# Performance work log

Hardware: AMD Instinct MI355X
Metric: run time of the kernel (lower is better)

## Reference

```python
import jax, jax.numpy as jnp
import numpy as np

W_CUB = 0.1
W_CD = 1.0
W_EXT = 0.01
W_SPS = 0.01
THRED = 24.0
COS_EPS = 1e-4

# cube face buffers (6 faces x 3 coords)
MASK_PROJECT = jnp.array([[0,1,1],[0,1,1],[1,0,1],[1,0,1],[1,1,0],[1,1,0]], jnp.float32)
MASK_PLANE   = jnp.array([[1,0,0],[1,0,0],[0,1,0],[0,1,0],[0,0,1],[0,0,1]], jnp.float32)
CUBE_NORMAL  = jnp.array([[-1,0,0],[1,0,0],[0,-1,0],[0,1,0],[0,0,-1],[0,0,1]], jnp.float32)
# torch repeat(...,3,...) of [[-1,-1,-1],[1,1,1]] tiles it -> [c0,c1,c0,c1,c0,c1]
CUBE_PLANES6 = jnp.tile(jnp.array([[-1.,-1.,-1.],[1.,1.,1.]], jnp.float32), (3,1))


def setup_inputs():
    B, P, N, S = 4, 24, 3072, 128
    key = jax.random.key(0)
    ks = jax.random.split(key, 8)
    pc_inver = jax.random.normal(ks[0], (B, P, N, 3), jnp.float32)
    normals_inver = jax.random.normal(ks[1], (B, P, N, 3), jnp.float32)
    scale = jax.random.uniform(ks[2], (B, P, 3), jnp.float32) * 0.9 + 0.1
    shape = jax.random.uniform(ks[3], (B, P, 2), jnp.float32) * 1.3 + 0.2
    exist = jax.random.uniform(ks[4], (B, P, 1), jnp.float32) * 0.98 + 0.01
    assign_matrix = jax.nn.softmax(jax.random.normal(ks[5], (B, N, P), jnp.float32), axis=-1)
    etas = jax.random.uniform(ks[6], (B, P, S), jnp.float32, minval=-jnp.pi/2, maxval=jnp.pi/2)
    omegas = jax.random.uniform(ks[7], (B, P, S), jnp.float32, minval=-jnp.pi, maxval=jnp.pi)
    return dict(pc_inver=pc_inver, normals_inver=normals_inver, scale=scale,
                shape=shape, exist=exist, assign_matrix=assign_matrix,
                etas=etas, omegas=omegas)


def _fexp(x, p):
    return jnp.sign(x) * jnp.abs(x) ** p


def _sample_sq_points(scale, eps, etas, omegas):
    # scale (B,P,3), eps (B,P,2), etas/omegas (B,P,S) -> (B,P,S,3)
    etas = jnp.where(etas == 0, 1e-6, etas)
    omegas = jnp.where(omegas == 0, 1e-6, omegas)
    a1, a2, a3 = scale[..., 0:1], scale[..., 1:2], scale[..., 2:3]
    e1, e2 = eps[..., 0:1], eps[..., 1:2]
    ce, se = jnp.cos(etas), jnp.sin(etas)
    co, so = jnp.cos(omegas), jnp.sin(omegas)
    x = a1 * _fexp(ce, e1) * _fexp(co, e2)
    y = a2 * _fexp(ce, e1) * _fexp(so, e2)
    z = a3 * _fexp(se, e1)
    fix = lambda v: (jnp.where(v > 0, 1.0, -1.0)) * jnp.maximum(jnp.abs(v), 1e-6)
    return jnp.stack([fix(x), fix(y), fix(z)], -1)


def _cd_loss(pc_inver, scale, shape, exist, assign_matrix, etas, omegas):
    X = _sample_sq_points(scale, shape, etas, omegas)          # (B,P,S,3)
    diff = X[:, :, :, None, :] - pc_inver[:, :, None, :, :]    # (B,P,S,N,3)
    D = jnp.sum(diff * diff, -1)                               # (B,P,S,N)
    pcl2prim = jnp.min(D, axis=2)                              # (B,P,N)
    pcl_loss = jnp.mean(jnp.sum(jnp.swapaxes(pcl2prim, 1, 2) * assign_matrix, -1))
    prim2pcl = jnp.mean(jnp.min(D, axis=3), axis=-1)           # (B,P)
    e = exist[..., 0]
    prim_loss = jnp.mean(jnp.sum(prim2pcl * e, -1) / (jnp.sum(e, -1) + 1e-6))
    return pcl_loss, prim_loss


def _cuboid_loss(pc_inver, normals_inver, scale, assign_matrix):
    pc = jnp.swapaxes(pc_inver, 1, 2)        # (B,N,P,3)
    nrm = jnp.swapaxes(normals_inver, 1, 2)  # (B,N,P,3)
    n_norm = jnp.maximum(jnp.linalg.norm(nrm, axis=-1, keepdims=True), COS_EPS)
    cos = jnp.einsum('bnpc,fc->bnpf', nrm, CUBE_NORMAL) / n_norm  # ||cube_normal||=1
    idx = jnp.argmax(cos, axis=-1)           # (B,N,P)
    s = scale[:, None, :, None, :]           # (B,1,P,1,3)
    proj = pc[:, :, :, None, :] * MASK_PROJECT + (CUBE_PLANES6 * s) * MASK_PLANE  # (B,N,P,6,3)
    proj = jnp.clip(proj, -s, s)
    proj_sel = jnp.take_along_axis(proj, idx[..., None, None], axis=3)[..., 0, :]  # (B,N,P,3)
    d = jnp.sum((proj_sel - pc) ** 2, -1)    # (B,N,P)
    return jnp.mean(jnp.sum(d * assign_matrix, -1))


def _common_losses(assign_matrix, exist):
    gt = jax.lax.stop_gradient((jnp.sum(assign_matrix, 1) > THRED).astype(jnp.float32))  # (B,P)
    p = exist[..., 0]
    bce = -jnp.mean(gt * jnp.log(p) + (1.0 - gt) * jnp.log1p(-p))
    N = assign_matrix.shape[1]
    sps = jnp.mean(jnp.mean(jnp.sqrt(jnp.sum(assign_matrix, 1) / N + 0.01), -1) ** 2)
    return bce, sps


def reference(pc_inver, normals_inver, scale, shape, exist, assign_matrix, etas, omegas):
    cub = _cuboid_loss(pc_inver, normals_inver, scale, assign_matrix)
    pcl_loss, prim_loss = _cd_loss(pc_inver, scale, shape, exist, assign_matrix, etas, omegas)
    bce, sps = _common_losses(assign_matrix, exist)
    return W_CUB * cub + W_CD * (pcl_loss + prim_loss) + W_EXT * bce + W_SPS * sps
```

## Files before the change

### kernel.cpp

```cpp
#include <hip/hip_runtime.h>
#include <math.h>

#define BB 4
#define PP 24
#define NN 3072
#define SS 128
#define CHUNK 512
#define NSPLIT 6
#define PART_STRIDE 132
#define FINF 3.4e38f

__device__ __forceinline__ float fexp_f(float v, float p) {
    float m = powf(fabsf(v), p);
    float s = (v > 0.f) ? 1.f : ((v < 0.f) ? -1.f : 0.f);
    return s * m;
}
__device__ __forceinline__ float fix_f(float v) {
    return ((v > 0.f) ? 1.f : -1.f) * fmaxf(fabsf(v), 1e-6f);
}
__device__ __forceinline__ float wave_sum(float v) {
    #pragma unroll
    for (int off = 32; off > 0; off >>= 1) v += __shfl_down(v, off);
    return v;
}
__device__ __forceinline__ float cub_dist(float px, float py, float pz,
                                          float nx, float ny, float nz,
                                          float sc0, float sc1, float sc2) {
    float best = -nx; int idx = 0;
    if ( nx > best) { best =  nx; idx = 1; }
    if (-ny > best) { best = -ny; idx = 2; }
    if ( ny > best) { best =  ny; idx = 3; }
    if (-nz > best) { best = -nz; idx = 4; }
    if ( nz > best) { best =  nz; idx = 5; }
    const int c = idx >> 1;
    const float scc = (c == 0) ? sc0 : ((c == 1) ? sc1 : sc2);
    const float fv  = (idx & 1) ? scc : -scc;
    float pr0 = (c == 0) ? fv : fminf(fmaxf(px, -sc0), sc0);
    float pr1 = (c == 1) ? fv : fminf(fmaxf(py, -sc1), sc1);
    float pr2 = (c == 2) ? fv : fminf(fmaxf(pz, -sc2), sc2);
    float d0 = pr0 - px, d1 = pr1 - py, d2 = pr2 - pz;
    return fmaf(d0, d0, fmaf(d1, d1, d2 * d2));
}

__global__ __launch_bounds__(256) void superdec_main(
    const float* __restrict__ pc, const float* __restrict__ nrm,
    const float* __restrict__ scale, const float* __restrict__ shape,
    const float* __restrict__ assign,
    const float* __restrict__ etas, const float* __restrict__ omegas,
    float* __restrict__ ws)
{
    const int blk   = blockIdx.x;
    const int bp    = blk / NSPLIT;
    const int split = blk % NSPLIT;
    const int b     = bp / PP;
    const int p     = bp % PP;
    const int tid   = threadIdx.x;
    const int n0    = split * CHUNK;
    const int pid   = tid & 127;
    const int q     = tid >> 7;

    __shared__ float4 Xs[SS];
    __shared__ float4 Pts[CHUNK];
    __shared__ float4 dmin2[2][128];
    __shared__ float  red[8 * SS];
    __shared__ float  wsum[6];

    const float sc0 = scale[bp * 3 + 0];
    const float sc1 = scale[bp * 3 + 1];
    const float sc2 = scale[bp * 3 + 2];

    const float4* pc4 = (const float4*)(pc + ((size_t)bp * NN + n0) * 3);
    const float4 g0 = pc4[pid * 3 + 0];
    const float4 g1 = pc4[pid * 3 + 1];
    const float4 g2 = pc4[pid * 3 + 2];
    const float px0 = g0.x, py0 = g0.y, pz0 = g0.z;
    const float px1 = g0.w, py1 = g1.x, pz1 = g1.y;
    const float px2 = g1.z, py2 = g1.w, pz2 = g2.x;
    const float px3 = g2.y, py3 = g2.z, pz3 = g2.w;
    const float ps0 = fmaf(px0, px0, fmaf(py0, py0, pz0 * pz0));
    const float ps1 = fmaf(px1, px1, fmaf(py1, py1, pz1 * pz1));
    const float ps2 = fmaf(px2, px2, fmaf(py2, py2, pz2 * pz2));
    const float ps3 = fmaf(px3, px3, fmaf(py3, py3, pz3 * pz3));

    float cub0 = 0.f, cub1 = 0.f, cub2 = 0.f, cub3 = 0.f;
    float am0 = 0.f, am1 = 0.f, am2 = 0.f, am3 = 0.f;

    if (q == 0) {
        {
            const float e1 = shape[bp * 2 + 0];
            const float e2 = shape[bp * 2 + 1];
            float eta = etas[bp * SS + tid];
            float omg = omegas[bp * SS + tid];
            eta = (eta == 0.f) ? 1e-6f : eta;
            omg = (omg == 0.f) ? 1e-6f : omg;
            float ce = cosf(eta), se = sinf(eta);
            float co = cosf(omg), so = sinf(omg);
            float fce = fexp_f(ce, e1);
            float x = fix_f(sc0 * fce * fexp_f(co, e2));
            float y = fix_f(sc1 * fce * fexp_f(so, e2));
            float z = fix_f(sc2 * fexp_f(se, e1));
            float xsq = fmaf(x, x, fmaf(y, y, z * z));
            Xs[tid] = make_float4(-2.f * x, -2.f * y, -2.f * z, xsq);
        }
        Pts[pid * 4 + 0] = make_float4(px0, py0, pz0, ps0);
        Pts[pid * 4 + 1] = make_float4(px1, py1, pz1, ps1);
        Pts[pid * 4 + 2] = make_float4(px2, py2, pz2, ps2);
        Pts[pid * 4 + 3] = make_float4(px3, py3, pz3, ps3);
        const float4* nr4 = (const float4*)(nrm + ((size_t)bp * NN + n0) * 3);
        const float4 h0 = nr4[pid * 3 + 0];
        const float4 h1 = nr4[pid * 3 + 1];
        const float4 h2 = nr4[pid * 3 + 2];
        cub0 = cub_dist(px0, py0, pz0, h0.x, h0.y, h0.z, sc0, sc1, sc2);
        cub1 = cub_dist(px1, py1, pz1, h0.w, h1.x, h1.y, sc0, sc1, sc2);
        cub2 = cub_dist(px2, py2, pz2, h1.z, h1.w, h2.x, sc0, sc1, sc2);
        cub3 = cub_dist(px3, py3, pz3, h2.y, h2.z, h2.w, sc0, sc1, sc2);
        const size_t abase = ((size_t)b * NN + n0 + pid * 4) * PP + p;
        am0 = assign[abase + 0 * PP];
        am1 = assign[abase + 1 * PP];
        am2 = assign[abase + 2 * PP];
        am3 = assign[abase + 3 * PP];
    }
    __syncthreads();

    {
        const int sb = q * 64;
        float m0 = FINF, m1 = FINF, m2 = FINF, m3 = FINF;
        #pragma unroll 4
        for (int s = 0; s < 64; s += 2) {
            float4 xa = Xs[sb + s];
            float4 xb = Xs[sb + s + 1];
            float d;
            d = fmaf(xa.x, px0, fmaf(xa.y, py0, fmaf(xa.z, pz0, xa.w))); m0 = fminf(m0, d);
            d = fmaf(xa.x, px1, fmaf(xa.y, py1, fmaf(xa.z, pz1, xa.w))); m1 = fminf(m1, d);
            d = fmaf(xa.x, px2, fmaf(xa.y, py2, fmaf(xa.z, pz2, xa.w))); m2 = fminf(m2, d);
            d = fmaf(xa.x, px3, fmaf(xa.y, py3, fmaf(xa.z, pz3, xa.w))); m3 = fminf(m3, d);
            d = fmaf(xb.x, px0, fmaf(xb.y, py0, fmaf(xb.z, pz0, xb.w))); m0 = fminf(m0, d);
            d = fmaf(xb.x, px1, fmaf(xb.y, py1, fmaf(xb.z, pz1, xb.w))); m1 = fminf(m1, d);
            d = fmaf(xb.x, px2, fmaf(xb.y, py2, fmaf(xb.z, pz2, xb.w))); m2 = fminf(m2, d);
            d = fmaf(xb.x, px3, fmaf(xb.y, py3, fmaf(xb.z, pz3, xb.w))); m3 = fminf(m3, d);
        }
        dmin2[q][pid] = make_float4(m0, m1, m2, m3);
    }
    __syncthreads();

    if (q == 0) {
        float4 a = dmin2[0][pid];
        float4 c = dmin2[1][pid];
        float d0 = fminf(a.x, c.x) + ps0;
        float d1 = fminf(a.y, c.y) + ps1;
        float d2 = fminf(a.z, c.z) + ps2;
        float d3 = fminf(a.w, c.w) + ps3;
        float acc_pcl = d0 * am0 + d1 * am1 + d2 * am2 + d3 * am3;
        float acc_cub = cub0 * am0 + cub1 * am1 + cub2 * am2 + cub3 * am3;
        float acc_am  = am0 + am1 + am2 + am3;
        float s0 = wave_sum(acc_pcl);
        float s1 = wave_sum(acc_cub);
        float s2 = wave_sum(acc_am);
        const int lane = tid & 63, wave = tid >> 6;
        if (lane == 0) {
            wsum[wave * 3 + 0] = s0;
            wsum[wave * 3 + 1] = s1;
            wsum[wave * 3 + 2] = s2;
        }
    }

    {
        const int rep = tid >> 5;
        const int sb  = tid & 31;
        const float4 x0 = Xs[sb];
        const float4 x1 = Xs[sb + 32];
        const float4 x2 = Xs[sb + 64];
        const float4 x3 = Xs[sb + 96];
        const int nb = rep * 64;
        float r0 = FINF, r1 = FINF, r2 = FINF, r3 = FINF;
        #pragma unroll 4
        for (int n = 0; n < 64; n += 2) {
            float4 pa = Pts[nb + n];
            float4 pb = Pts[nb + n + 1];
            float d;
            d = fmaf(x0.x, pa.x, fmaf(x0.y, pa.y, fmaf(x0.z, pa.z, pa.w))); r0 = fminf(r0, d);
            d = fmaf(x1.x, pa.x, fmaf(x1.y, pa.y, fmaf(x1.z, pa.z, pa.w))); r1 = fminf(r1, d);
            d = fmaf(x2.x, pa.x, fmaf(x2.y, pa.y, fmaf(x2.z, pa.z, pa.w))); r2 = fminf(r2, d);
            d = fmaf(x3.x, pa.x, fmaf(x3.y, pa.y, fmaf(x3.z, pa.z, pa.w))); r3 = fminf(r3, d);
            d = fmaf(x0.x, pb.x, fmaf(x0.y, pb.y, fmaf(x0.z, pb.z, pb.w))); r0 = fminf(r0, d);
            d = fmaf(x1.x, pb.x, fmaf(x1.y, pb.y, fmaf(x1.z, pb.z, pb.w))); r1 = fminf(r1, d);
            d = fmaf(x2.x, pb.x, fmaf(x2.y, pb.y, fmaf(x2.z, pb.z, pb.w))); r2 = fminf(r2, d);
            d = fmaf(x3.x, pb.x, fmaf(x3.y, pb.y, fmaf(x3.z, pb.z, pb.w))); r3 = fminf(r3, d);
        }
        red[rep * SS + sb +  0] = r0;
        red[rep * SS + sb + 32] = r1;
        red[rep * SS + sb + 64] = r2;
        red[rep * SS + sb + 96] = r3;
    }
    __syncthreads();

    float* part = ws + (size_t)(bp * NSPLIT + split) * PART_STRIDE;
    if (tid < SS) {
        float m = red[tid];
        #pragma unroll
        for (int r = 1; r < 8; ++r) m = fminf(m, red[r * SS + tid]);
        part[tid] = m + Xs[tid].w;
    }
    if (tid == 0) {
        part[SS + 0] = wsum[0] + wsum[3];
        part[SS + 1] = wsum[1] + wsum[4];
        part[SS + 2] = wsum[2] + wsum[5];
    }
}

__global__ __launch_bounds__(1024) void superdec_reduce_final(
    const float* __restrict__ ws, const float* __restrict__ exist,
    float* __restrict__ out)
{
    __shared__ float s_prim[96];
    __shared__ float s_pcl[96], s_cub[96], s_bce[96], s_e[96], s_sq[96];
    const int t    = threadIdx.x;
    const int lane = t & 63;
    if (t < 96) s_prim[t] = 0.f;
    __syncthreads();

    #pragma unroll
    for (int k = 0; k < (96 * 128) / 1024; ++k) {
        const int idx = t + k * 1024;
        const int bp  = idx >> 7;
        const int s   = idx & 127;
        const float* base = ws + (size_t)bp * (NSPLIT * PART_STRIDE) + s;
        float m = fminf(fminf(fminf(base[0 * PART_STRIDE], base[1 * PART_STRIDE]),
                              fminf(base[2 * PART_STRIDE], base[3 * PART_STRIDE])),
                        fminf(base[4 * PART_STRIDE], base[5 * PART_STRIDE]));
        float sm = wave_sum(m);
        if (lane == 0) atomicAdd(&s_prim[bp], sm);
    }

    if (t < 96) {
        const float* base = ws + (size_t)t * (NSPLIT * PART_STRIDE) + SS;
        float pcl = 0.f, cub = 0.f, cs = 0.f;
        #pragma unroll
        for (int sp = 0; sp < NSPLIT; ++sp) {
            pcl += base[sp * PART_STRIDE + 0];
            cub += base[sp * PART_STRIDE + 1];
            cs  += base[sp * PART_STRIDE + 2];
        }
        const float e  = exist[t];
        const float gt = (cs > 24.0f) ? 1.f : 0.f;
        s_pcl[t] = pcl;
        s_cub[t] = cub;
        s_bce[t] = gt * logf(e) + (1.f - gt) * log1pf(-e);
        s_e[t]   = e;
        s_sq[t]  = sqrtf(cs / (float)NN + 0.01f);
    }
    __syncthreads();

    if (t == 0) {
        float pcl_sum = 0.f, cub_sum = 0.f, bce_sum = 0.f, prim_loss = 0.f, sps = 0.f;
        #pragma unroll
        for (int b_ = 0; b_ < BB; ++b_) {
            float pe = 0.f, ee = 0.f, sq = 0.f;
            #pragma unroll
            for (int p_ = 0; p_ < PP; ++p_) {
                const int i = b_ * PP + p_;
                pcl_sum += s_pcl[i];
                cub_sum += s_cub[i];
                bce_sum += s_bce[i];
                pe += (s_prim[i] / (float)SS) * s_e[i];
                ee += s_e[i];
                sq += s_sq[i];
            }
            prim_loss += pe / (ee + 1e-6f);
            float mb = sq / (float)PP;
            sps += mb * mb;
        }
        prim_loss /= (float)BB;
        sps       /= (float)BB;
        float pcl_loss = pcl_sum / (float)(BB * NN);
        float cub      = cub_sum / (float)(BB * NN);
        float bce      = -bce_sum / (float)(BB * PP);
        out[0] = 0.1f * cub + 1.0f * (pcl_loss + prim_loss) + 0.01f * bce + 0.01f * sps;
    }
}

extern "C" void kernel_launch(void* const* d_in, const int* in_sizes, int n_in,
                              void* d_out, int out_size, void* d_ws, size_t ws_size,
                              hipStream_t stream) {
    const float* pc     = (const float*)d_in[0];
    const float* nrm    = (const float*)d_in[1];
    const float* scale  = (const float*)d_in[2];
    const float* shape  = (const float*)d_in[3];
    const float* exist  = (const float*)d_in[4];
    const float* assign = (const float*)d_in[5];
    const float* etas   = (const float*)d_in[6];
    const float* omegas = (const float*)d_in[7];
    float* ws  = (float*)d_ws;
    float* out = (float*)d_out;

    superdec_main<<<BB * PP * NSPLIT, 256, 0, stream>>>(
        pc, nrm, scale, shape, assign, etas, omegas, ws);
    superdec_reduce_final<<<1, 1024, 0, stream>>>(ws, exist, out);
}
```

Baseline: 94.61 us.

## Fuse final reduction into main kernel via last-block atomic counter

Replaces the separate single-block reduce kernel with a last-block-done pattern: each block bumps a global atomic counter after a threadfence, and the final block performs the cross-block reduction. The per-split minima layout is changed to an interleaved [bp*128+s][8] format so the reducer reads two float4s per entry. A tiny zeroing kernel is launched to reset the counter, so the launch count stays at two. The intent is to drop the dependent reduce launch's latency and make its global reads coalesced, at the cost of serialized tail work in one block plus atomic and fence overhead.

```diff
diff --git a/kernel.cpp b/kernel.cpp
--- a/kernel.cpp
+++ b/kernel.cpp
@@ -7,8 +7,11 @@
 #define SS 128
 #define CHUNK 512
 #define NSPLIT 6
-#define PART_STRIDE 132
+#define GRID (BB * PP * NSPLIT)
 #define FINF 3.4e38f
+
+#define SCAL_F (96 * 128 * 8)
+#define CNT_F  (SCAL_F + 96 * 6 * 4)
 
 __device__ __forceinline__ float fexp_f(float v, float p) {
     float m = powf(fabsf(v), p);
@@ -42,12 +45,16 @@
     return fmaf(d0, d0, fmaf(d1, d1, d2 * d2));
 }
 
-__global__ __launch_bounds__(256) void superdec_main(
+__global__ void superdec_zero(float* __restrict__ ws) {
+    *(unsigned int*)(ws + CNT_F) = 0u;
+}
+
+__global__ __launch_bounds__(256) void superdec_fused(
     const float* __restrict__ pc, const float* __restrict__ nrm,
     const float* __restrict__ scale, const float* __restrict__ shape,
-    const float* __restrict__ assign,
+    const float* __restrict__ exist, const float* __restrict__ assign,
     const float* __restrict__ etas, const float* __restrict__ omegas,
-    float* __restrict__ ws)
+    float* __restrict__ ws, float* __restrict__ out)
 {
     const int blk   = blockIdx.x;
     const int bp    = blk / NSPLIT;
@@ -64,6 +71,7 @@
     __shared__ float4 dmin2[2][128];
     __shared__ float  red[8 * SS];
     __shared__ float  wsum[6];
+    __shared__ unsigned int s_flag;
 
     const float sc0 = scale[bp * 3 + 0];
     const float sc1 = scale[bp * 3 + 1];
@@ -156,8 +164,8 @@
         float s0 = wave_sum(acc_pcl);
         float s1 = wave_sum(acc_cub);
         float s2 = wave_sum(acc_am);
-        const int lane = tid & 63, wave = tid >> 6;
-        if (lane == 0) {
+        const int lane_ = tid & 63, wave = tid >> 6;
+        if (lane_ == 0) {
             wsum[wave * 3 + 0] = s0;
             wsum[wave * 3 + 1] = s1;
             wsum[wave * 3 + 2] = s2;
@@ -194,64 +202,62 @@
     }
     __syncthreads();
 
-    float* part = ws + (size_t)(bp * NSPLIT + split) * PART_STRIDE;
     if (tid < SS) {
         float m = red[tid];
         #pragma unroll
         for (int r = 1; r < 8; ++r) m = fminf(m, red[r * SS + tid]);
-        part[tid] = m + Xs[tid].w;
+        ws[(size_t)(bp * SS + tid) * 8 + split] = m + Xs[tid].w;
     }
     if (tid == 0) {
-        part[SS + 0] = wsum[0] + wsum[3];
-        part[SS + 1] = wsum[1] + wsum[4];
-        part[SS + 2] = wsum[2] + wsum[5];
-    }
-}
-
-__global__ __launch_bounds__(1024) void superdec_reduce_final(
-    const float* __restrict__ ws, const float* __restrict__ exist,
-    float* __restrict__ out)
-{
-    __shared__ float s_prim[96];
-    __shared__ float s_pcl[96], s_cub[96], s_bce[96], s_e[96], s_sq[96];
-    const int t    = threadIdx.x;
-    const int lane = t & 63;
-    if (t < 96) s_prim[t] = 0.f;
-    __syncthreads();
-
-    #pragma unroll
-    for (int k = 0; k < (96 * 128) / 1024; ++k) {
-        const int idx = t + k * 1024;
-        const int bp  = idx >> 7;
-        const int s   = idx & 127;
-        const float* base = ws + (size_t)bp * (NSPLIT * PART_STRIDE) + s;
-        float m = fminf(fminf(fminf(base[0 * PART_STRIDE], base[1 * PART_STRIDE]),
-                              fminf(base[2 * PART_STRIDE], base[3 * PART_STRIDE])),
-                        fminf(base[4 * PART_STRIDE], base[5 * PART_STRIDE]));
+        float* sc = ws + SCAL_F + (bp * NSPLIT + split) * 4;
+        sc[0] = wsum[0] + wsum[3];
+        sc[1] = wsum[1] + wsum[4];
+        sc[2] = wsum[2] + wsum[5];
+    }
+
+    __syncthreads();
+    if (tid == 0) {
+        __threadfence();
+        s_flag = atomicAdd((unsigned int*)(ws + CNT_F), 1u);
+    }
+    __syncthreads();
+    if (s_flag != (unsigned int)(GRID - 1)) return;
+    __threadfence();
+
+    if (tid < 96) red[tid] = 0.f;
+    __syncthreads();
+
+    const int lane = tid & 63;
+    #pragma unroll 4
+    for (int k = 0; k < 48; ++k) {
+        const int idx = tid + (k << 8);
+        const float4* m4 = ((const float4*)ws) + (idx << 1);
+        const float4 a  = m4[0];
+        const float4 b2 = m4[1];
+        float m = fminf(fminf(fminf(a.x, a.y), fminf(a.z, a.w)), fminf(b2.x, b2.y));
         float sm = wave_sum(m);
-        if (lane == 0) atomicAdd(&s_prim[bp], sm);
-    }
-
-    if (t < 96) {
-        const float* base = ws + (size_t)t * (NSPLIT * PART_STRIDE) + SS;
-        float pcl = 0.f, cub = 0.f, cs = 0.f;
+        if (lane == 0) atomicAdd(&red[idx >> 7], sm);
+    }
+    if (tid < 96) {
+        const float* sc = ws + SCAL_F + tid * (NSPLIT * 4);
+        float pcl = 0.f, cubv = 0.f, cs = 0.f;
         #pragma unroll
         for (int sp = 0; sp < NSPLIT; ++sp) {
-            pcl += base[sp * PART_STRIDE + 0];
-            cub += base[sp * PART_STRIDE + 1];
-            cs  += base[sp * PART_STRIDE + 2];
-        }
-        const float e  = exist[t];
+            pcl  += sc[sp * 4 + 0];
+            cubv += sc[sp * 4 + 1];
+            cs   += sc[sp * 4 + 2];
+        }
+        const float e  = exist[tid];
         const float gt = (cs > 24.0f) ? 1.f : 0.f;
-        s_pcl[t] = pcl;
-        s_cub[t] = cub;
-        s_bce[t] = gt * logf(e) + (1.f - gt) * log1pf(-e);
-        s_e[t]   = e;
-        s_sq[t]  = sqrtf(cs / (float)NN + 0.01f);
-    }
-    __syncthreads();
-
-    if (t == 0) {
+        red[ 96 + tid] = pcl;
+        red[192 + tid] = cubv;
+        red[288 + tid] = gt * logf(e) + (1.f - gt) * log1pf(-e);
+        red[384 + tid] = e;
+        red[480 + tid] = sqrtf(cs / (float)NN + 0.01f);
+    }
+    __syncthreads();
+
+    if (tid == 0) {
         float pcl_sum = 0.f, cub_sum = 0.f, bce_sum = 0.f, prim_loss = 0.f, sps = 0.f;
         #pragma unroll
         for (int b_ = 0; b_ < BB; ++b_) {
@@ -259,12 +265,12 @@
             #pragma unroll
             for (int p_ = 0; p_ < PP; ++p_) {
                 const int i = b_ * PP + p_;
-                pcl_sum += s_pcl[i];
-                cub_sum += s_cub[i];
-                bce_sum += s_bce[i];
-                pe += (s_prim[i] / (float)SS) * s_e[i];
-                ee += s_e[i];
-                sq += s_sq[i];
+                pcl_sum += red[ 96 + i];
+                cub_sum += red[192 + i];
+                bce_sum += red[288 + i];
+                pe += (red[i] / (float)SS) * red[384 + i];
+                ee += red[384 + i];
+                sq += red[480 + i];
             }
             prim_loss += pe / (ee + 1e-6f);
             float mb = sq / (float)PP;
@@ -273,9 +279,9 @@
         prim_loss /= (float)BB;
         sps       /= (float)BB;
         float pcl_loss = pcl_sum / (float)(BB * NN);
-        float cub      = cub_sum / (float)(BB * NN);
+        float cubf     = cub_sum / (float)(BB * NN);
         float bce      = -bce_sum / (float)(BB * PP);
-        out[0] = 0.1f * cub + 1.0f * (pcl_loss + prim_loss) + 0.01f * bce + 0.01f * sps;
+        out[0] = 0.1f * cubf + 1.0f * (pcl_loss + prim_loss) + 0.01f * bce + 0.01f * sps;
     }
 }
 
@@ -293,7 +299,8 @@
     float* ws  = (float*)d_ws;
     float* out = (float*)d_out;
 
-    superdec_main<<<BB * PP * NSPLIT, 256, 0, stream>>>(
-        pc, nrm, scale, shape, assign, etas, omegas, ws);
-    superdec_reduce_final<<<1, 1024, 0, stream>>>(ws, exist, out);
-}
+    superdec_zero<<<1, 1, 0, stream>>>(ws);
+
+    superdec_fused<<<GRID, 256, 0, stream>>>(
+        pc, nrm, scale, shape, exist, assign, etas, omegas, ws, out);
+}
```

After: 123.4 us. 1.3x slower.
